# Optimization experiments

Measured on AMD Instinct MI355X. Metric: run time of the kernel, lower is better.

## Reference

```python
import jax, jax.numpy as jnp
import numpy as np

DIM = 1024
NUM_HEADS = 8
HEAD_DIM = 128
MAX_SEQ_LEN = 2048
ATTN_SCALE = 0.12
RMS_EPS = 1.1920929e-07  # torch float32 eps (F.rms_norm default)


def rms_norm(x):
    return x * jax.lax.rsqrt(jnp.mean(jnp.square(x), axis=-1, keepdims=True) + RMS_EPS)


def rope_tables(T):
    # angular_freq: (1/1024)**linspace(0,1,head_dim//4), padded with head_dim//4 zeros -> length head_dim//2
    af = (1.0 / 1024.0) ** np.linspace(0.0, 1.0, HEAD_DIM // 4, dtype=np.float32)
    af = np.concatenate([af, np.zeros(HEAD_DIM // 4, dtype=np.float32)])
    t = np.arange(T, dtype=np.float32)
    theta = np.einsum('i,j->ij', t, af)  # [T, head_dim//2]
    return jnp.asarray(np.cos(theta)), jnp.asarray(np.sin(theta))


def apply_rope(x_BTHD, cos, sin):
    # cos/sin: [T, head_dim//2] -> broadcast [1,T,1,hd//2]
    c = cos[None, :, None, :]
    s = sin[None, :, None, :]
    x1, x2 = jnp.split(x_BTHD, 2, axis=-1)
    y1 = x1 * c + x2 * s
    y2 = -x1 * s + x2 * c
    return jnp.concatenate([y1, y2], axis=-1)


def setup_inputs() -> dict:
    key = jax.random.key(0)
    k1, k2, k3, k4, k5 = jax.random.split(key, 5)
    B, T = 4, 2048
    hdim = NUM_HEADS * HEAD_DIM
    std = 0.5 * DIM ** (-0.5)
    bound = (3.0 ** 0.5) * std
    x = jax.random.normal(k1, (B, T, DIM), dtype=jnp.float32)
    ve = jax.random.normal(k2, (B, T, DIM), dtype=jnp.float32)
    sa_lambdas = jax.random.uniform(k3, (2,), dtype=jnp.float32)
    qkv_w = jax.random.uniform(k4, (3, hdim, DIM), dtype=jnp.float32, minval=-bound, maxval=bound)
    # original inits c_proj to zeros; use small random so the output is non-trivial
    c_proj_weight = jax.random.normal(k5, (DIM, hdim), dtype=jnp.float32) * 0.02
    return {"x": x, "ve": ve, "sa_lambdas": sa_lambdas, "qkv_w": qkv_w,
            "c_proj_weight": c_proj_weight}


def reference(x, ve, sa_lambdas, qkv_w, c_proj_weight):
    B, T, D = x.shape
    H, hd = NUM_HEADS, HEAD_DIM
    Wqkv = qkv_w.reshape(3 * H * hd, D)
    qkv = jnp.einsum('btd,ed->bte', x, Wqkv).reshape(B, T, 3 * H, hd)
    q, k, v = jnp.split(qkv, 3, axis=-2)  # each [B,T,H,hd]
    q, k = rms_norm(q), rms_norm(k)
    cos, sin = rope_tables(T)
    q, k = apply_rope(q, cos, sin), apply_rope(k, cos, sin)
    v = sa_lambdas[0] * v + sa_lambdas[1] * ve.reshape(B, T, H, hd)
    # [B,H,T,T] scores
    attn = jnp.einsum('bqhd,bkhd->bhqk', q, k) * ATTN_SCALE
    causal = jnp.triu(jnp.ones((T, T), dtype=bool), k=1)
    attn = jnp.where(causal[None, None], -jnp.inf, attn)
    attn = jax.nn.softmax(attn, axis=-1)
    y = jnp.einsum('bhqk,bkhd->bqhd', attn, v).reshape(B, T, H * hd)
    return jnp.einsum('bte,de->btd', y, c_proj_weight)
```

## Files before the change

kernel.cpp:

```cpp
#include <hip/hip_runtime.h>

#define DIM 1024
#define NH 8
#define HD 128
#define T_SEQ 2048
#define NTOK 8192
#define QKV_N 3072
#define ATTN_SCALE 0.12f
#define RMS_EPS 1.1920929e-07f

using f32x4  = __attribute__((ext_vector_type(4))) float;
using bf16x8 = __attribute__((ext_vector_type(8))) __bf16;

__device__ __forceinline__ unsigned short f2bf(float f) {
    unsigned int u = __builtin_bit_cast(unsigned int, f);
    u += 0x7fffu + ((u >> 16) & 1u);
    return (unsigned short)(u >> 16);
}
__device__ __forceinline__ float bf2f(unsigned short s) {
    unsigned int u = ((unsigned int)s) << 16;
    return __builtin_bit_cast(float, u);
}

__device__ __forceinline__ void gll16(const void* g, void* l) {
    __builtin_amdgcn_global_load_lds(
        (const __attribute__((address_space(1))) unsigned int*)g,
        (__attribute__((address_space(3))) unsigned int*)l, 16, 0, 0);
}

__global__ __launch_bounds__(256) void cvt_f32_bf16(const float* __restrict__ in,
                                                    unsigned short* __restrict__ out,
                                                    int n4) {
    int i = blockIdx.x * 256 + threadIdx.x;
    if (i < n4) {
        float4 f = ((const float4*)in)[i];
        ushort4 o;
        o.x = f2bf(f.x); o.y = f2bf(f.y); o.z = f2bf(f.z); o.w = f2bf(f.w);
        ((ushort4*)out)[i] = o;
    }
}

template<int OUTF32>
__global__ __launch_bounds__(256) void gemm_bt(const unsigned short* __restrict__ A,
                                               const unsigned short* __restrict__ B,
                                               void* __restrict__ Cout,
                                               int M, int N, int K) {
    __shared__ unsigned short lA[128*32];
    __shared__ unsigned short lB[128*32];
    const int tid  = threadIdx.x;
    const int lane = tid & 63;
    const int w    = tid >> 6;
    const int wm   = w >> 1, wn = w & 1;
    const int lr   = lane & 15, lg = lane >> 4;
    const int m0   = blockIdx.y * 128;
    const int n0   = blockIdx.x * 128;
    const int srow = lane >> 2;
    const int scol = (lane & 3) * 8;

    f32x4 acc[4][4] = {};

    for (int k0 = 0; k0 < K; k0 += 32) {
        __syncthreads();
        #pragma unroll
        for (int i = 0; i < 2; ++i) {
            int c = w*2 + i;
            gll16(&A[(size_t)(m0 + c*16 + srow)*K + k0 + scol], &lA[c*512]);
            gll16(&B[(size_t)(n0 + c*16 + srow)*K + k0 + scol], &lB[c*512]);
        }
        __syncthreads();
        bf16x8 af[4], bfr[4];
        #pragma unroll
        for (int i = 0; i < 4; ++i)
            af[i]  = *(const bf16x8*)&lA[(wm*64 + i*16 + lr)*32 + lg*8];
        #pragma unroll
        for (int j = 0; j < 4; ++j)
            bfr[j] = *(const bf16x8*)&lB[(wn*64 + j*16 + lr)*32 + lg*8];
        #pragma unroll
        for (int i = 0; i < 4; ++i)
            #pragma unroll
            for (int j = 0; j < 4; ++j)
                acc[i][j] = __builtin_amdgcn_mfma_f32_16x16x32_bf16(af[i], bfr[j], acc[i][j], 0, 0, 0);
    }

    #pragma unroll
    for (int i = 0; i < 4; ++i)
        #pragma unroll
        for (int j = 0; j < 4; ++j)
            #pragma unroll
            for (int r = 0; r < 4; ++r) {
                int row = m0 + wm*64 + i*16 + lg*4 + r;
                int col = n0 + wn*64 + j*16 + lr;
                if (OUTF32) ((float*)Cout)[(size_t)row*N + col] = acc[i][j][r];
                else ((unsigned short*)Cout)[(size_t)row*N + col] = f2bf(acc[i][j][r]);
            }
}

__global__ __launch_bounds__(256) void qkv_post(const unsigned short* __restrict__ qkv,
                                                unsigned short* __restrict__ qO,
                                                unsigned short* __restrict__ kO) {
    int gw   = (blockIdx.x * 256 + threadIdx.x) >> 6;
    int lane = threadIdx.x & 63;
    int h     = gw & 7;
    int token = gw >> 3;
    int t     = token & (T_SEQ-1);
    int b     = token >> 11;

    const unsigned short* base = qkv + (size_t)token * QKV_N + h*HD;
    float q1 = bf2f(base[lane]),        q2 = bf2f(base[lane+64]);
    float k1 = bf2f(base[1024+lane]),   k2 = bf2f(base[1024+lane+64]);

    float sq = q1*q1 + q2*q2;
    float sk = k1*k1 + k2*k2;
    #pragma unroll
    for (int m = 1; m < 64; m <<= 1) {
        sq += __shfl_xor(sq, m);
        sk += __shfl_xor(sk, m);
    }
    float qs = rsqrtf(sq * (1.0f/128.0f) + RMS_EPS) * ATTN_SCALE;
    float ks = rsqrtf(sk * (1.0f/128.0f) + RMS_EPS);
    q1 *= qs; q2 *= qs; k1 *= ks; k2 *= ks;

    float theta = (lane < 32) ? (float)t * exp2f((float)lane * (-10.0f/31.0f)) : 0.0f;
    float sn, cs;
    sincosf(theta, &sn, &cs);
    float qy1 =  q1*cs + q2*sn, qy2 = -q1*sn + q2*cs;
    float ky1 =  k1*cs + k2*sn, ky2 = -k1*sn + k2*cs;

    size_t obase = ((size_t)(b*NH + h) * T_SEQ + t) * HD;
    qO[obase + lane]      = f2bf(qy1);
    qO[obase + lane + 64] = f2bf(qy2);
    kO[obase + lane]      = f2bf(ky1);
    kO[obase + lane + 64] = f2bf(ky2);
}

__global__ __launch_bounds__(256) void vmix_t(const unsigned short* __restrict__ qkv,
                                              const float* __restrict__ ve,
                                              const float* __restrict__ lam,
                                              unsigned short* __restrict__ vt) {
    __shared__ unsigned short lT[128*72];
    const int tid = threadIdx.x;
    const int t0  = blockIdx.x * 64;
    const int bh  = blockIdx.y;
    const int b = bh >> 3, h = bh & 7;
    const float l0 = lam[0], l1 = lam[1];

    #pragma unroll
    for (int it = 0; it < 4; ++it) {
        int g  = it*256 + tid;
        int t  = g >> 4;
        int d8 = (g & 15) << 3;
        size_t token = (size_t)b*T_SEQ + t0 + t;
        ushort4 v0 = *(const ushort4*)&qkv[token*QKV_N + 2048 + h*HD + d8];
        ushort4 v1 = *(const ushort4*)&qkv[token*QKV_N + 2048 + h*HD + d8 + 4];
        float4 e0 = *(const float4*)&ve[token*DIM + h*HD + d8];
        float4 e1 = *(const float4*)&ve[token*DIM + h*HD + d8 + 4];
        lT[(d8+0)*72 + t] = f2bf(l0*bf2f(v0.x) + l1*e0.x);
        lT[(d8+1)*72 + t] = f2bf(l0*bf2f(v0.y) + l1*e0.y);
        lT[(d8+2)*72 + t] = f2bf(l0*bf2f(v0.z) + l1*e0.z);
        lT[(d8+3)*72 + t] = f2bf(l0*bf2f(v0.w) + l1*e0.w);
        lT[(d8+4)*72 + t] = f2bf(l0*bf2f(v1.x) + l1*e1.x);
        lT[(d8+5)*72 + t] = f2bf(l0*bf2f(v1.y) + l1*e1.y);
        lT[(d8+6)*72 + t] = f2bf(l0*bf2f(v1.z) + l1*e1.z);
        lT[(d8+7)*72 + t] = f2bf(l0*bf2f(v1.w) + l1*e1.w);
    }
    __syncthreads();
    #pragma unroll
    for (int it = 0; it < 4; ++it) {
        int g  = it*256 + tid;
        int d  = g >> 3;
        int t8 = (g & 7) << 3;
        uint4 pk = *(const uint4*)&lT[d*72 + t8];
        *(uint4*)&vt[((size_t)bh*HD + d)*T_SEQ + t0 + t8] = pk;
    }
}

__global__ __launch_bounds__(256) void attn_fwd(const unsigned short* __restrict__ Q,
                                                const unsigned short* __restrict__ K,
                                                const unsigned short* __restrict__ Vt,
                                                unsigned short* __restrict__ Y) {
    __shared__ unsigned short lK[64*128];
    __shared__ unsigned short lV[128*64];
    __shared__ unsigned short lP[4][16*72];

    const int tid  = threadIdx.x;
    const int lane = tid & 63;
    const int w    = tid >> 6;
    const int lr   = lane & 15, lg = lane >> 4;

    const int lin = blockIdx.y * 16 + blockIdx.x;
    const int bh  = (lin & 7)*4 + ((lin >> 3) & 3);
    const int p   = lin >> 5;
    const int qtA = p, qtB = 31 - p;

    const unsigned short* Qg = Q  + (size_t)bh * T_SEQ * HD;
    const unsigned short* Kg = K  + (size_t)bh * T_SEQ * HD;
    const unsigned short* Vg = Vt + (size_t)bh * HD * T_SEQ;
    const int q0A = qtA*64 + w*16;
    const int q0B = qtB*64 + w*16;

    bf16x8 qfA[4], qfB[4];
    #pragma unroll
    for (int kk = 0; kk < 4; ++kk) {
        qfA[kk] = *(const bf16x8*)&Qg[(size_t)(q0A + lr)*HD + kk*32 + lg*8];
        qfB[kk] = *(const bf16x8*)&Qg[(size_t)(q0B + lr)*HD + kk*32 + lg*8];
    }

    f32x4 oA[8] = {}, oB[8] = {};
    float psA[4] = {0.f,0.f,0.f,0.f}, psB[4] = {0.f,0.f,0.f,0.f};

    auto pass = [&](const bf16x8* qf, f32x4* o, float* ps, int q0, bool diag, int kbase) {
        f32x4 sf[4];
        #pragma unroll
        for (int j = 0; j < 4; ++j) {
            f32x4 s = {0.f,0.f,0.f,0.f};
            #pragma unroll
            for (int kk = 0; kk < 4; ++kk) {
                bf16x8 kf = *(const bf16x8*)&lK[(j*16+lr)*128 + ((kk*32 + lg*8) ^ ((lr&7)<<3))];
                s = __builtin_amdgcn_mfma_f32_16x16x32_bf16(qf[kk], kf, s, 0, 0, 0);
            }
            sf[j] = s;
        }
        if (diag) {
            #pragma unroll
            for (int j = 0; j < 4; ++j)
                #pragma unroll
                for (int r = 0; r < 4; ++r) {
                    int kcol = kbase + j*16 + lr;
                    int qrow = q0 + lg*4 + r;
                    if (kcol > qrow) sf[j][r] = -INFINITY;
                }
        }
        #pragma unroll
        for (int j = 0; j < 4; ++j)
            #pragma unroll
            for (int r = 0; r < 4; ++r) {
                float pp = __expf(sf[j][r]);
                sf[j][r] = pp;
                ps[r] += pp;
            }
        #pragma unroll
        for (int j = 0; j < 4; ++j)
            #pragma unroll
            for (int r = 0; r < 4; ++r)
                lP[w][(lg*4+r)*72 + j*16 + lr] = f2bf(sf[j][r]);
        asm volatile("" ::: "memory");
        bf16x8 pf0 = *(const bf16x8*)&lP[w][lr*72 + lg*8];
        bf16x8 pf1 = *(const bf16x8*)&lP[w][lr*72 + 32 + lg*8];
        #pragma unroll
        for (int n = 0; n < 8; ++n) {
            bf16x8 vf0 = *(const bf16x8*)&lV[(n*16+lr)*64 + (( 0 + lg*8) ^ ((lr&7)<<3))];
            o[n] = __builtin_amdgcn_mfma_f32_16x16x32_bf16(pf0, vf0, o[n], 0, 0, 0);
            bf16x8 vf1 = *(const bf16x8*)&lV[(n*16+lr)*64 + ((32 + lg*8) ^ ((lr&7)<<3))];
            o[n] = __builtin_amdgcn_mfma_f32_16x16x32_bf16(pf1, vf1, o[n], 0, 0, 0);
        }
    };

    for (int kt = 0; kt <= qtB; ++kt) {
        const int kbase = kt * 64;
        __syncthreads();
        #pragma unroll
        for (int i = 0; i < 4; ++i) {
            int c = w*4 + i;
            {
                int row = c*4 + (lane >> 4);
                int col = ((lane & 15) << 3) ^ ((row & 7) << 3);
                gll16(&Kg[(size_t)(kbase + row)*HD + col], &lK[c*512]);
            }
            {
                int row = c*8 + (lane >> 3);
                int col = ((lane & 7) << 3) ^ ((row & 7) << 3);
                gll16(&Vg[(size_t)row*T_SEQ + kbase + col], &lV[c*512]);
            }
        }
        __syncthreads();
        if (kt <= qtA) pass(qfA, oA, psA, q0A, kt == qtA, kbase);
        pass(qfB, oB, psB, q0B, kt == qtB, kbase);
    }

    #pragma unroll
    for (int m = 1; m < 16; m <<= 1)
        #pragma unroll
        for (int r = 0; r < 4; ++r) {
            psA[r] += __shfl_xor(psA[r], m);
            psB[r] += __shfl_xor(psB[r], m);
        }

    const int b = bh >> 3, h = bh & 7;
    #pragma unroll
    for (int n = 0; n < 8; ++n)
        #pragma unroll
        for (int r = 0; r < 4; ++r) {
            int d = n*16 + lr;
            int qrowA = q0A + lg*4 + r;
            int qrowB = q0B + lg*4 + r;
            Y[((size_t)(b*T_SEQ + qrowA))*DIM + h*HD + d] = f2bf(oA[n][r] / psA[r]);
            Y[((size_t)(b*T_SEQ + qrowB))*DIM + h*HD + d] = f2bf(oB[n][r] / psB[r]);
        }
}

extern "C" void kernel_launch(void* const* d_in, const int* in_sizes, int n_in,
                              void* d_out, int out_size, void* d_ws, size_t ws_size,
                              hipStream_t stream) {
    const float* x      = (const float*)d_in[0];
    const float* ve     = (const float*)d_in[1];
    const float* lam    = (const float*)d_in[2];
    const float* qkvw   = (const float*)d_in[3];
    const float* cprojw = (const float*)d_in[4];

    char* ws = (char*)d_ws;
    unsigned short* xb  = (unsigned short*)(ws);
    unsigned short* wqb = (unsigned short*)(ws + 16777216);
    unsigned short* cpb = (unsigned short*)(ws + 23068672);
    unsigned short* qkv = (unsigned short*)(ws + 25165824);
    unsigned short* qa  = (unsigned short*)(ws + 75497472);
    unsigned short* ka  = (unsigned short*)(ws + 92274688);
    unsigned short* vt  = (unsigned short*)(ws + 109051904);
    unsigned short* ya  = (unsigned short*)(ws + 125829120);

    cvt_f32_bf16<<<8192, 256, 0, stream>>>(x, xb, 2097152);
    cvt_f32_bf16<<<3072, 256, 0, stream>>>(qkvw, wqb, 786432);
    cvt_f32_bf16<<<1024, 256, 0, stream>>>(cprojw, cpb, 262144);

    gemm_bt<0><<<dim3(24, 64), 256, 0, stream>>>(xb, wqb, qkv, NTOK, QKV_N, DIM);
    qkv_post<<<16384, 256, 0, stream>>>(qkv, qa, ka);
    vmix_t<<<dim3(32, 32), 256, 0, stream>>>(qkv, ve, lam, vt);
    attn_fwd<<<dim3(16, 32), 256, 0, stream>>>(qa, ka, vt, ya);
    gemm_bt<1><<<dim3(8, 64), 256, 0, stream>>>(ya, cpb, (float*)d_out, NTOK, DIM, DIM);
}
```

Before: 209.0 us.

## Rewrite GEMMs as 256x128 triple-buffered kernels and double-buffer attention K/V loads

Replaces the 128x128 single-buffered GEMM with a 512-thread 256x128x64 kernel. It uses triple-buffered LDS with async global-to-LDS loads, vmcnt-based waits, XOR swizzling, an XCD-aware block remap, setprio around MFMAs and an LDS-staged vectorized epilogue. The attention kernel gets double-buffered K/V tiles with a single barrier per iteration, a swizzled P buffer and a reciprocal-multiply normalization. The aim is to overlap memory latency with MFMA work and cut barrier and bank-conflict stalls. The cost is heavy LDS use (one block per CU for the GEMM) and fragile hand-managed waitcnt ordering.

After: 202.1 us. 3.3% less time.

```diff
diff --git a/kernel.cpp b/kernel.cpp
--- a/kernel.cpp
+++ b/kernel.cpp
@@ -27,6 +27,8 @@
         (const __attribute__((address_space(1))) unsigned int*)g,
         (__attribute__((address_space(3))) unsigned int*)l, 16, 0, 0);
 }
+
+#define VMCNT(n) asm volatile("s_waitcnt vmcnt(" #n ")" ::: "memory")
 
 __global__ __launch_bounds__(256) void cvt_f32_bf16(const float* __restrict__ in,
                                                     unsigned short* __restrict__ out,
@@ -40,59 +42,126 @@
     }
 }
 
+#define GBM 256
+#define GBN 128
+#define GBK 64
+#define SLOT_A 32768
+#define SLOT_SZ 49152
+
 template<int OUTF32>
-__global__ __launch_bounds__(256) void gemm_bt(const unsigned short* __restrict__ A,
-                                               const unsigned short* __restrict__ B,
-                                               void* __restrict__ Cout,
-                                               int M, int N, int K) {
-    __shared__ unsigned short lA[128*32];
-    __shared__ unsigned short lB[128*32];
+__global__ __launch_bounds__(512, 1) void gemm256(const unsigned short* __restrict__ A,
+                                                  const unsigned short* __restrict__ B,
+                                                  void* __restrict__ Cout,
+                                                  int M, int N, int K, int nbn) {
+    __shared__ __align__(16) char smem[147456];
     const int tid  = threadIdx.x;
     const int lane = tid & 63;
     const int w    = tid >> 6;
     const int wm   = w >> 1, wn = w & 1;
     const int lr   = lane & 15, lg = lane >> 4;
-    const int m0   = blockIdx.y * 128;
-    const int n0   = blockIdx.x * 128;
-    const int srow = lane >> 2;
-    const int scol = (lane & 3) * 8;
-
-    f32x4 acc[4][4] = {};
-
-    for (int k0 = 0; k0 < K; k0 += 32) {
-        __syncthreads();
+    const int xsw  = (lr & 7) << 3;
+
+    const int chunk = gridDim.x >> 3;
+    const int bid2  = (blockIdx.x & 7) * chunk + (blockIdx.x >> 3);
+    const int m0 = (bid2 / nbn) * GBM;
+    const int n0 = (bid2 % nbn) * GBN;
+
+    const int rsub = lane >> 3;
+    const int csw  = ((lane & 7) ^ rsub) << 3;
+
+    char* s0 = smem;
+    char* s1 = smem + SLOT_SZ;
+    char* s2 = smem + 2*SLOT_SZ;
+
+    auto stage = [&](int kt, char* slot) {
+        const int kb = kt * GBK;
+        #pragma unroll
+        for (int i = 0; i < 4; ++i) {
+            int c = w*4 + i;
+            gll16(&A[(size_t)(m0 + c*8 + rsub)*K + kb + csw], slot + c*1024);
+        }
         #pragma unroll
         for (int i = 0; i < 2; ++i) {
             int c = w*2 + i;
-            gll16(&A[(size_t)(m0 + c*16 + srow)*K + k0 + scol], &lA[c*512]);
-            gll16(&B[(size_t)(n0 + c*16 + srow)*K + k0 + scol], &lB[c*512]);
-        }
-        __syncthreads();
-        bf16x8 af[4], bfr[4];
-        #pragma unroll
-        for (int i = 0; i < 4; ++i)
-            af[i]  = *(const bf16x8*)&lA[(wm*64 + i*16 + lr)*32 + lg*8];
-        #pragma unroll
-        for (int j = 0; j < 4; ++j)
-            bfr[j] = *(const bf16x8*)&lB[(wn*64 + j*16 + lr)*32 + lg*8];
-        #pragma unroll
-        for (int i = 0; i < 4; ++i)
-            #pragma unroll
-            for (int j = 0; j < 4; ++j)
-                acc[i][j] = __builtin_amdgcn_mfma_f32_16x16x32_bf16(af[i], bfr[j], acc[i][j], 0, 0, 0);
-    }
-
-    #pragma unroll
-    for (int i = 0; i < 4; ++i)
-        #pragma unroll
-        for (int j = 0; j < 4; ++j)
-            #pragma unroll
-            for (int r = 0; r < 4; ++r) {
-                int row = m0 + wm*64 + i*16 + lg*4 + r;
-                int col = n0 + wn*64 + j*16 + lr;
-                if (OUTF32) ((float*)Cout)[(size_t)row*N + col] = acc[i][j][r];
-                else ((unsigned short*)Cout)[(size_t)row*N + col] = f2bf(acc[i][j][r]);
-            }
+            gll16(&B[(size_t)(n0 + c*8 + rsub)*K + kb + csw], slot + SLOT_A + c*1024);
+        }
+    };
+
+    f32x4 acc[4][4] = {};
+    const int KT = K / GBK;
+
+    stage(0, s0);
+    stage(1, s1);
+    VMCNT(6);
+    __builtin_amdgcn_s_barrier();
+    __builtin_amdgcn_sched_barrier(0);
+
+    for (int t = 0; t < KT; ++t) {
+        if (t + 2 < KT) stage(t + 2, s2);
+        const unsigned short* sA = (const unsigned short*)s0;
+        const unsigned short* sB = (const unsigned short*)(s0 + SLOT_A);
+        bf16x8 bfr[4][2];
+        #pragma unroll
+        for (int n = 0; n < 4; ++n)
+            #pragma unroll
+            for (int kk = 0; kk < 2; ++kk)
+                bfr[n][kk] = *(const bf16x8*)&sB[(wn*64 + n*16 + lr)*64 + ((kk*32 + lg*8) ^ xsw)];
+        #pragma unroll
+        for (int m = 0; m < 4; ++m) {
+            bf16x8 af[2];
+            #pragma unroll
+            for (int kk = 0; kk < 2; ++kk)
+                af[kk] = *(const bf16x8*)&sA[(wm*64 + m*16 + lr)*64 + ((kk*32 + lg*8) ^ xsw)];
+            __builtin_amdgcn_s_setprio(1);
+            #pragma unroll
+            for (int n = 0; n < 4; ++n)
+                #pragma unroll
+                for (int kk = 0; kk < 2; ++kk)
+                    acc[m][n] = __builtin_amdgcn_mfma_f32_16x16x32_bf16(af[kk], bfr[n][kk], acc[m][n], 0, 0, 0);
+            __builtin_amdgcn_s_setprio(0);
+        }
+        if (t + 2 < KT) { VMCNT(6); }
+        else            { VMCNT(0); }
+        __builtin_amdgcn_s_barrier();
+        __builtin_amdgcn_sched_barrier(0);
+        char* tmp = s0; s0 = s1; s1 = s2; s2 = tmp;
+    }
+
+    __syncthreads();
+    float* sc = (float*)(smem + (size_t)w * 17408);
+    #pragma unroll
+    for (int m = 0; m < 4; ++m)
+        #pragma unroll
+        for (int n = 0; n < 4; ++n)
+            #pragma unroll
+            for (int r = 0; r < 4; ++r)
+                sc[(m*16 + lg*4 + r)*68 + n*16 + lr] = acc[m][n][r];
+
+    if (OUTF32) {
+        float* C = (float*)Cout;
+        #pragma unroll
+        for (int rnd = 0; rnd < 16; ++rnd) {
+            int g = rnd*64 + lane;
+            int row = g >> 4, c4 = (g & 15) * 4;
+            float4 v = *(float4*)&sc[row*68 + c4];
+            *(float4*)&C[(size_t)(m0 + wm*64 + row)*N + n0 + wn*64 + c4] = v;
+        }
+    } else {
+        unsigned short* C = (unsigned short*)Cout;
+        #pragma unroll
+        for (int rnd = 0; rnd < 8; ++rnd) {
+            int g = rnd*64 + lane;
+            int row = g >> 3, c8 = (g & 7) * 8;
+            float4 v0 = *(float4*)&sc[row*68 + c8];
+            float4 v1 = *(float4*)&sc[row*68 + c8 + 4];
+            uint4 o;
+            o.x = f2bf(v0.x) | ((unsigned)f2bf(v0.y) << 16);
+            o.y = f2bf(v0.z) | ((unsigned)f2bf(v0.w) << 16);
+            o.z = f2bf(v1.x) | ((unsigned)f2bf(v1.y) << 16);
+            o.w = f2bf(v1.z) | ((unsigned)f2bf(v1.w) << 16);
+            *(uint4*)&C[(size_t)(m0 + wm*64 + row)*N + n0 + wn*64 + c8] = o;
+        }
+    }
 }
 
 __global__ __launch_bounds__(256) void qkv_post(const unsigned short* __restrict__ qkv,
@@ -178,9 +247,9 @@
                                                 const unsigned short* __restrict__ K,
                                                 const unsigned short* __restrict__ Vt,
                                                 unsigned short* __restrict__ Y) {
-    __shared__ unsigned short lK[64*128];
-    __shared__ unsigned short lV[128*64];
-    __shared__ unsigned short lP[4][16*72];
+    __shared__ unsigned short lK[2][64*128];
+    __shared__ unsigned short lV[2][128*64];
+    __shared__ unsigned short lP[4][16*64];
 
     const int tid  = threadIdx.x;
     const int lane = tid & 63;
@@ -198,26 +267,51 @@
     const int q0A = qtA*64 + w*16;
     const int q0B = qtB*64 + w*16;
 
+    auto stage = [&](int kt, int s) {
+        const int kbase = kt * 64;
+        #pragma unroll
+        for (int i = 0; i < 4; ++i) {
+            int c = w*4 + i;
+            int row = c*4 + (lane >> 4);
+            int col = ((lane & 15) << 3) ^ ((row & 7) << 3);
+            gll16(&Kg[(size_t)(kbase + row)*HD + col], &lK[s][c*512]);
+        }
+        #pragma unroll
+        for (int i = 0; i < 4; ++i) {
+            int c = w*4 + i;
+            int row = c*8 + (lane >> 3);
+            int col = ((lane & 7) << 3) ^ ((row & 7) << 3);
+            gll16(&Vg[(size_t)row*T_SEQ + kbase + col], &lV[s][c*512]);
+        }
+    };
+
     bf16x8 qfA[4], qfB[4];
     #pragma unroll
     for (int kk = 0; kk < 4; ++kk) {
         qfA[kk] = *(const bf16x8*)&Qg[(size_t)(q0A + lr)*HD + kk*32 + lg*8];
         qfB[kk] = *(const bf16x8*)&Qg[(size_t)(q0B + lr)*HD + kk*32 + lg*8];
     }
+    VMCNT(0);
+    #pragma unroll
+    for (int kk = 0; kk < 4; ++kk)
+        asm volatile("" :: "v"(qfA[kk]), "v"(qfB[kk]));
 
     f32x4 oA[8] = {}, oB[8] = {};
     float psA[4] = {0.f,0.f,0.f,0.f}, psB[4] = {0.f,0.f,0.f,0.f};
 
-    auto pass = [&](const bf16x8* qf, f32x4* o, float* ps, int q0, bool diag, int kbase) {
+    auto pass = [&](const bf16x8* qf, f32x4* o, float* ps, int q0, bool diag,
+                    int kbase, const unsigned short* lKc, const unsigned short* lVc) {
         f32x4 sf[4];
         #pragma unroll
         for (int j = 0; j < 4; ++j) {
             f32x4 s = {0.f,0.f,0.f,0.f};
+            __builtin_amdgcn_s_setprio(1);
             #pragma unroll
             for (int kk = 0; kk < 4; ++kk) {
-                bf16x8 kf = *(const bf16x8*)&lK[(j*16+lr)*128 + ((kk*32 + lg*8) ^ ((lr&7)<<3))];
+                bf16x8 kf = *(const bf16x8*)&lKc[(j*16+lr)*128 + ((kk*32 + lg*8) ^ ((lr&7)<<3))];
                 s = __builtin_amdgcn_mfma_f32_16x16x32_bf16(qf[kk], kf, s, 0, 0, 0);
             }
+            __builtin_amdgcn_s_setprio(0);
             sf[j] = s;
         }
         if (diag) {
@@ -241,40 +335,40 @@
         #pragma unroll
         for (int j = 0; j < 4; ++j)
             #pragma unroll
-            for (int r = 0; r < 4; ++r)
-                lP[w][(lg*4+r)*72 + j*16 + lr] = f2bf(sf[j][r]);
+            for (int r = 0; r < 4; ++r) {
+                int prow = lg*4 + r;
+                lP[w][prow*64 + ((j*16 + lr) ^ ((prow&7)<<3))] = f2bf(sf[j][r]);
+            }
         asm volatile("" ::: "memory");
-        bf16x8 pf0 = *(const bf16x8*)&lP[w][lr*72 + lg*8];
-        bf16x8 pf1 = *(const bf16x8*)&lP[w][lr*72 + 32 + lg*8];
+        bf16x8 pf[2];
+        #pragma unroll
+        for (int kk = 0; kk < 2; ++kk)
+            pf[kk] = *(const bf16x8*)&lP[w][lr*64 + ((kk*32 + lg*8) ^ ((lr&7)<<3))];
         #pragma unroll
         for (int n = 0; n < 8; ++n) {
-            bf16x8 vf0 = *(const bf16x8*)&lV[(n*16+lr)*64 + (( 0 + lg*8) ^ ((lr&7)<<3))];
-            o[n] = __builtin_amdgcn_mfma_f32_16x16x32_bf16(pf0, vf0, o[n], 0, 0, 0);
-            bf16x8 vf1 = *(const bf16x8*)&lV[(n*16+lr)*64 + ((32 + lg*8) ^ ((lr&7)<<3))];
-            o[n] = __builtin_amdgcn_mfma_f32_16x16x32_bf16(pf1, vf1, o[n], 0, 0, 0);
+            __builtin_amdgcn_s_setprio(1);
+            #pragma unroll
+            for (int kk = 0; kk < 2; ++kk) {
+                bf16x8 vf = *(const bf16x8*)&lVc[(n*16+lr)*64 + ((kk*32 + lg*8) ^ ((lr&7)<<3))];
+                o[n] = __builtin_amdgcn_mfma_f32_16x16x32_bf16(pf[kk], vf, o[n], 0, 0, 0);
+            }
+            __builtin_amdgcn_s_setprio(0);
         }
     };
 
+    stage(0, 0);
     for (int kt = 0; kt <= qtB; ++kt) {
+        __builtin_amdgcn_s_barrier();
+        const bool pre = (kt + 1 <= qtB);
+        if (pre) stage(kt + 1, (kt + 1) & 1);
+        if (pre) { VMCNT(8); }
+        else     { VMCNT(0); }
+        __builtin_amdgcn_sched_barrier(0);
         const int kbase = kt * 64;
-        __syncthreads();
-        #pragma unroll
-        for (int i = 0; i < 4; ++i) {
-            int c = w*4 + i;
-            {
-                int row = c*4 + (lane >> 4);
-                int col = ((lane & 15) << 3) ^ ((row & 7) << 3);
-                gll16(&Kg[(size_t)(kbase + row)*HD + col], &lK[c*512]);
-            }
-            {
-                int row = c*8 + (lane >> 3);
-                int col = ((lane & 7) << 3) ^ ((row & 7) << 3);
-                gll16(&Vg[(size_t)row*T_SEQ + kbase + col], &lV[c*512]);
-            }
-        }
-        __syncthreads();
-        if (kt <= qtA) pass(qfA, oA, psA, q0A, kt == qtA, kbase);
-        pass(qfB, oB, psB, q0B, kt == qtB, kbase);
+        const unsigned short* lKc = lK[kt & 1];
+        const unsigned short* lVc = lV[kt & 1];
+        if (kt <= qtA) pass(qfA, oA, psA, q0A, kt == qtA, kbase, lKc, lVc);
+        pass(qfB, oB, psB, q0B, kt == qtB, kbase, lKc, lVc);
     }
 
     #pragma unroll
@@ -284,6 +378,9 @@
             psA[r] += __shfl_xor(psA[r], m);
             psB[r] += __shfl_xor(psB[r], m);
         }
+    float riA[4], riB[4];
+    #pragma unroll
+    for (int r = 0; r < 4; ++r) { riA[r] = 1.0f / psA[r]; riB[r] = 1.0f / psB[r]; }
 
     const int b = bh >> 3, h = bh & 7;
     #pragma unroll
@@ -293,8 +390,8 @@
             int d = n*16 + lr;
             int qrowA = q0A + lg*4 + r;
             int qrowB = q0B + lg*4 + r;
-            Y[((size_t)(b*T_SEQ + qrowA))*DIM + h*HD + d] = f2bf(oA[n][r] / psA[r]);
-            Y[((size_t)(b*T_SEQ + qrowB))*DIM + h*HD + d] = f2bf(oB[n][r] / psB[r]);
+            Y[((size_t)(b*T_SEQ + qrowA))*DIM + h*HD + d] = f2bf(oA[n][r] * riA[r]);
+            Y[((size_t)(b*T_SEQ + qrowB))*DIM + h*HD + d] = f2bf(oB[n][r] * riB[r]);
         }
 }
 
@@ -321,9 +418,9 @@
     cvt_f32_bf16<<<3072, 256, 0, stream>>>(qkvw, wqb, 786432);
     cvt_f32_bf16<<<1024, 256, 0, stream>>>(cprojw, cpb, 262144);
 
-    gemm_bt<0><<<dim3(24, 64), 256, 0, stream>>>(xb, wqb, qkv, NTOK, QKV_N, DIM);
+    gemm256<0><<<768, 512, 0, stream>>>(xb, wqb, qkv, NTOK, QKV_N, DIM, 24);
     qkv_post<<<16384, 256, 0, stream>>>(qkv, qa, ka);
     vmix_t<<<dim3(32, 32), 256, 0, stream>>>(qkv, ve, lam, vt);
     attn_fwd<<<dim3(16, 32), 256, 0, stream>>>(qa, ka, vt, ya);
-    gemm_bt<1><<<dim3(8, 64), 256, 0, stream>>>(ya, cpb, (float*)d_out, NTOK, DIM, DIM);
-}
+    gemm256<1><<<256, 512, 0, stream>>>(ya, cpb, (float*)d_out, NTOK, DIM, DIM, 8);
+}
```
